# Performance work log

Measured on AMD Instinct MI355X. Metric: run time of the kernel, lower is better.

Reference implementation:

```python
import jax, jax.numpy as jnp
import numpy as np

# dims: B=32 batch, F=40 max_frames, NB=36 num_boxes, R=512 region size, H=512 hidden
# feat_size D = R + 2H = 1536 ; relation attn input = 2D = 3072

def _soft_attention(feats, hidden, Wf, bf, Wh, bh, wa):
    # feats: (N, L, Din), hidden: (N, H) -> att feat (N, Din), alpha (N, L)
    e = jnp.tanh(feats @ Wf.T + bf + (hidden @ Wh.T + bh)[:, None, :]) @ wa  # (N, L)
    alpha = jax.nn.softmax(e, axis=1)
    att = jnp.einsum('nl,nld->nd', alpha, feats)
    return att, alpha


def setup_inputs() -> dict:
    key = jax.random.key(0)
    ks = jax.random.split(key, 16)
    B, F, NB, R, H = 32, 40, 36, 512, 512
    D = R + 2 * H  # 1536
    s = 0.02
    inp = {
        'i3d_feats': jax.random.normal(ks[0], (B, F, 2 * H), jnp.float32),
        'object_feats': jax.random.normal(ks[1], (B, F, NB, R), jnp.float32),
        'hidden_state': jax.random.normal(ks[2], (B, H), jnp.float32),
        # spatial SoftAttention(R, H, H)
        'Ws_f': jax.random.normal(ks[3], (H, R), jnp.float32) * s,
        'bs_f': jnp.zeros((H,), jnp.float32),
        'Ws_h': jax.random.normal(ks[4], (H, H), jnp.float32) * s,
        'bs_h': jnp.zeros((H,), jnp.float32),
        'was': jax.random.normal(ks[5], (H,), jnp.float32) * s,
        # relation SoftAttention(2D, H, H)
        'Wr_f': jax.random.normal(ks[6], (H, 2 * D), jnp.float32) * s,
        'br_f': jnp.zeros((H,), jnp.float32),
        'Wr_h': jax.random.normal(ks[7], (H, H), jnp.float32) * s,
        'br_h': jnp.zeros((H,), jnp.float32),
        'war': jax.random.normal(ks[8], (H,), jnp.float32) * s,
    }
    return inp


def reference(i3d_feats, object_feats, hidden_state,
              Ws_f, bs_f, Ws_h, bs_h, was,
              Wr_f, br_f, Wr_h, br_h, war):
    B, F, NB, R = object_feats.shape
    # ---- spatial attention over boxes (per frame) ----
    feats = object_feats.reshape(B * F, NB, R)
    hidden_rep = jnp.repeat(hidden_state, F, axis=0)  # == hidden.repeat(1,F).reshape(B*F,-1)
    obj_att, _ = _soft_attention(feats, hidden_rep, Ws_f, bs_f, Ws_h, bs_h, was)
    obj_att = obj_att.reshape(B, F, R)
    feat = jnp.concatenate([obj_att, i3d_feats], axis=-1)  # (B, F, D)
    D = feat.shape[-1]
    # ---- relation attention over all F*F frame pairs ----
    # pairwise[b, i*F + j] = concat(feat[b, j], feat[b, i])  (feat1 varies fast, feat2 slow)
    # Decompose Wr_f @ concat(fj, fi) = Wr1 @ fj + Wr2 @ fi to avoid O(F^2 * 2D) tensor.
    Wr1, Wr2 = Wr_f[:, :D], Wr_f[:, D:]
    p1 = feat @ Wr1.T  # (B, F, H), applied to fast index j
    p2 = feat @ Wr2.T  # (B, F, H), applied to slow index i
    hproj = hidden_state @ Wr_h.T + br_h  # (B, H)
    e = jnp.tanh(p2[:, :, None, :] + p1[:, None, :, :] + (hproj + br_f)[:, None, None, :]) @ war  # (B,F,F) [i,j]
    alpha = jax.nn.softmax(e.reshape(B, F * F), axis=1).reshape(B, F, F)
    # weighted sum of concat(feat[j], feat[i]) splits into two marginal sums
    rel1 = jnp.einsum('bij,bjd->bd', alpha, feat)
    rel2 = jnp.einsum('bij,bid->bd', alpha, feat)
    return jnp.concatenate([rel1, rel2], axis=-1)  # (B, 2D)
```

## Files before the change

kernel.cpp:

```cpp
#include <hip/hip_runtime.h>
#include <stdint.h>

#define B_SZ 32
#define F_SZ 40
#define NB_SZ 36
#define R_SZ 512
#define H_SZ 512
#define D_SZ 1536
#define M1 (B_SZ * F_SZ * NB_SZ)
#define NROW (B_SZ * F_SZ)
#define FNB (F_SZ * NB_SZ)

typedef __attribute__((ext_vector_type(8))) short short8;
typedef __attribute__((ext_vector_type(4))) float f32x4;

__device__ __forceinline__ unsigned short f2bf(float f) {
    unsigned int x = __float_as_uint(f);
    return (unsigned short)((x + 0x7fffu + ((x >> 16) & 1u)) >> 16);
}
__device__ __forceinline__ float bf2f(unsigned short u) {
    union { unsigned int i; float f; } v; v.i = ((unsigned int)u) << 16; return v.f;
}
__device__ __forceinline__ unsigned int cvtpk(float lo, float hi) {
    unsigned int r;
    asm("v_cvt_pk_bf16_f32 %0, %1, %2" : "=v"(r) : "v"(lo), "v"(hi));
    return r;
}
__device__ __forceinline__ float fast_rcp(float x) {
    float r; asm("v_rcp_f32 %0, %1" : "=v"(r) : "v"(x)); return r;
}
__device__ __forceinline__ float fast_tanh(float x) {
    float t = __builtin_amdgcn_exp2f(2.8853900817779268f * x);
    return 1.0f - 2.0f * fast_rcp(t + 1.0f);
}

__device__ __forceinline__ void gload_lds16(const void* gsrc, void* ldst) {
    __builtin_amdgcn_global_load_lds(
        (const __attribute__((address_space(1))) unsigned int*)gsrc,
        (__attribute__((address_space(3))) unsigned int*)ldst, 16, 0, 0);
}

__global__ __launch_bounds__(256) void k_pre(
    const float* __restrict__ hidden,
    const float* __restrict__ Wsh, const float* __restrict__ bsh,
    const float* __restrict__ bsf,
    const float* __restrict__ Wrh, const float* __restrict__ brh,
    const float* __restrict__ brf,
    float* __restrict__ hs, float* __restrict__ hr,
    const float* __restrict__ Wsf, unsigned short* __restrict__ Wsb)
{
    const int t = threadIdx.x;
    if (blockIdx.x >= 256) {
        int i = ((blockIdx.x - 256) * 256 + t) * 8;
        float4 f0 = *(const float4*)(Wsf + i);
        float4 f1 = *(const float4*)(Wsf + i + 4);
        uint4 pk = {cvtpk(f0.x, f0.y), cvtpk(f0.z, f0.w),
                    cvtpk(f1.x, f1.y), cvtpk(f1.z, f1.w)};
        *(uint4*)(Wsb + i) = pk;
        return;
    }
    __shared__ float hid[H_SZ];
    const int b = blockIdx.x >> 3, hc = blockIdx.x & 7;
    for (int i = t; i < H_SZ; i += 256) hid[i] = hidden[b * H_SZ + i];
    __syncthreads();
    const int h = hc * 64 + (t >> 2), kq = t & 3;
    const float* r1 = Wsh + (size_t)h * H_SZ + kq * 128;
    const float* r2 = Wrh + (size_t)h * H_SZ + kq * 128;
    const float* hh = hid + kq * 128;
    float a1 = 0.f, a2 = 0.f;
    for (int k = 0; k < 128; k += 4) {
        float4 v1 = *(const float4*)(r1 + k);
        float4 v2 = *(const float4*)(r2 + k);
        a1 += hh[k] * v1.x + hh[k+1] * v1.y + hh[k+2] * v1.z + hh[k+3] * v1.w;
        a2 += hh[k] * v2.x + hh[k+1] * v2.y + hh[k+2] * v2.z + hh[k+3] * v2.w;
    }
    a1 += __shfl_xor(a1, 1); a1 += __shfl_xor(a1, 2);
    a2 += __shfl_xor(a2, 1); a2 += __shfl_xor(a2, 2);
    if (kq == 0) {
        hs[b * H_SZ + h] = a1 + bsh[h] + bsf[h];
        hr[b * H_SZ + h] = a2 + brh[h] + brf[h];
    }
}

__global__ __launch_bounds__(256, 3) void k_e1_mfma(
    const float* __restrict__ feats,
    const unsigned short* __restrict__ Wsb,
    const float* __restrict__ was,
    const float* __restrict__ hs,
    float* __restrict__ e1p)
{
    __shared__ __align__(16) unsigned char As[2][64 * 128];
    __shared__ __align__(16) unsigned char Bs[2][128 * 128];
    __shared__ float hsl[2][256];
    __shared__ float wasl[256];
    __shared__ float eps[2][64];

    const int bx = blockIdx.x;
    const int wid = (bx & 7) * 180 + (bx >> 3);
    const int mb = wid >> 1, by = wid & 1;
    const int m0 = mb * 64, hb = by * 256;
    const int t = threadIdx.x;
    const int b0 = m0 / FNB, b1 = (m0 + 63) / FNB;
    const int thr = (b0 + 1) * FNB - m0;

    if (t < 256) {
        hsl[0][t] = hs[b0 * H_SZ + hb + t];
        hsl[1][t] = hs[b1 * H_SZ + hb + t];
        wasl[t]   = was[hb + t];
    }

    const int lane = t & 63, w = t >> 6;
    const int wr = w >> 1, wc = w & 1;
    const int l15 = lane & 15, lk = lane >> 4;

    int ar[2], brw[4];
#pragma unroll
    for (int i = 0; i < 2; i++) ar[i] = wr * 32 + i * 16 + l15;
#pragma unroll
    for (int j = 0; j < 4; j++) brw[j] = wc * 64 + j * 16 + l15;

    const int srow = t >> 3;
    const int scol = t & 7;
    const int wub  = (t & 192) * 16;

    float4 alo[2], ahi[2];
    f32x4 acc[2][8] = {};
    float ep[2][4] = {{0.f}};

#define E1_LOAD_A(K0) do { \
    _Pragma("unroll") \
    for (int it = 0; it < 2; it++) { \
        int cid = it * 256 + t; \
        int r = cid >> 3, c = cid & 7; \
        const float* src = feats + (size_t)(m0 + r) * R_SZ + (K0) + c * 8; \
        alo[it] = *(const float4*)src; \
        ahi[it] = *(const float4*)(src + 4); \
    } } while (0)

#define E1_WRITE_A(AB) do { \
    _Pragma("unroll") \
    for (int it = 0; it < 2; it++) { \
        int cid = it * 256 + t; \
        int r = cid >> 3, c = cid & 7; \
        uint4 pk = {cvtpk(alo[it].x, alo[it].y), cvtpk(alo[it].z, alo[it].w), \
                    cvtpk(ahi[it].x, ahi[it].y), cvtpk(ahi[it].z, ahi[it].w)}; \
        *(uint4*)(&As[AB][r * 128 + ((c ^ (r & 7)) << 4)]) = pk; \
    } } while (0)

#define E1_STAGE_B(BUF, HP, K0) do { \
    _Pragma("unroll") \
    for (int it = 0; it < 4; it++) { \
        int r = it * 32 + srow; \
        int gc = scol ^ (r & 7); \
        gload_lds16(Wsb + (size_t)(hb + (HP) * 128 + r) * R_SZ + (K0) + gc * 8, \
                    &Bs[BUF][it * 4096 + wub]); \
    } } while (0)

#define E1_COMPUTE(HP, BB, AB) do { \
    _Pragma("unroll") \
    for (int ks = 0; ks < 2; ks++) { \
        short8 a[2], bv[4]; \
        int c = ks * 4 + lk; \
        _Pragma("unroll") \
        for (int i = 0; i < 2; i++) \
            a[i] = *(const short8*)(&As[AB][ar[i] * 128 + ((c ^ (ar[i] & 7)) << 4)]); \
        _Pragma("unroll") \
        for (int j = 0; j < 4; j++) \
            bv[j] = *(const short8*)(&Bs[BB][brw[j] * 128 + ((c ^ (brw[j] & 7)) << 4)]); \
        _Pragma("unroll") \
        for (int i = 0; i < 2; i++) \
        _Pragma("unroll") \
        for (int j = 0; j < 4; j++) \
            acc[i][(HP) * 4 + j] = __builtin_amdgcn_mfma_f32_16x16x32_bf16( \
                a[i], bv[j], acc[i][(HP) * 4 + j], 0, 0, 0); \
    } } while (0)

    E1_LOAD_A(0);
    E1_STAGE_B(0, 0, 0);
    E1_WRITE_A(0);
    __syncthreads();

    for (int ki = 0; ki < 8; ki++) {
        const int ab = ki & 1;
        E1_STAGE_B(1, 1, ki * 64);
        if (ki < 7) E1_LOAD_A((ki + 1) * 64);
        E1_COMPUTE(0, 0, ab);
        __syncthreads();
        if (ki < 7) E1_STAGE_B(0, 0, (ki + 1) * 64);
        E1_COMPUTE(1, 1, ab);
        if (ki < 7) E1_WRITE_A(ab ^ 1);
        __syncthreads();
    }

#pragma unroll
    for (int jj = 0; jj < 8; jj++) {
        int hl = (jj >> 2) * 128 + wc * 64 + (jj & 3) * 16 + l15;
        float wv = wasl[hl];
#pragma unroll
        for (int i = 0; i < 2; i++) {
#pragma unroll
            for (int q = 0; q < 4; q++) {
                int r = wr * 32 + i * 16 + lk * 4 + q;
                float hv = hsl[r >= thr ? 1 : 0][hl];
                ep[i][q] += fast_tanh(acc[i][jj][q] + hv) * wv;
            }
        }
    }
#pragma unroll
    for (int i = 0; i < 2; i++)
#pragma unroll
        for (int q = 0; q < 4; q++) {
            float v = ep[i][q];
            v += __shfl_xor(v, 1);
            v += __shfl_xor(v, 2);
            v += __shfl_xor(v, 4);
            v += __shfl_xor(v, 8);
            if (l15 == 0) eps[wc][wr * 32 + i * 16 + lk * 4 + q] = v;
        }
    __syncthreads();
    if (t < 64) e1p[(size_t)by * M1 + m0 + t] = eps[0][t] + eps[1][t];
#undef E1_LOAD_A
#undef E1_WRITE_A
#undef E1_STAGE_B
#undef E1_COMPUTE
}

__global__ __launch_bounds__(256) void k_softatt(
    const float* __restrict__ feats,
    const float* __restrict__ i3d,
    const float* __restrict__ e1p,
    unsigned short* __restrict__ feat)
{
    __shared__ float alpha[2][NB_SZ];
    const int n0 = blockIdx.x * 2;
    const int t = threadIdx.x;
    const int w = t >> 6;

    if (w < 2) {
        const int n = n0 + w, lane = t & 63;
        float v = -1e30f;
        if (lane < NB_SZ) {
            int idx = n * NB_SZ + lane;
            v = e1p[idx] + e1p[M1 + idx];
        }
        float m = v;
#pragma unroll
        for (int off = 32; off; off >>= 1) m = fmaxf(m, __shfl_xor(m, off));
        float ex = (lane < NB_SZ) ? __expf(v - m) : 0.f;
        float ssum = ex;
#pragma unroll
        for (int off = 32; off; off >>= 1) ssum += __shfl_xor(ssum, off);
        if (lane < NB_SZ) alpha[w][lane] = ex / ssum;
    }
    __syncthreads();

    const int g = t >> 7, lc = t & 127;
    const int n = n0 + g;
    float4 a4 = {0.f, 0.f, 0.f, 0.f};
    const float* base = feats + (size_t)n * NB_SZ * R_SZ + lc * 4;
    for (int ll = 0; ll < NB_SZ; ll++) {
        float al = alpha[g][ll];
        float4 pv = *(const float4*)(base + ll * R_SZ);
        a4.x += al * pv.x; a4.y += al * pv.y;
        a4.z += al * pv.z; a4.w += al * pv.w;
    }
    uint2 att = {cvtpk(a4.x, a4.y), cvtpk(a4.z, a4.w)};
    *(uint2*)(feat + (size_t)n * D_SZ + lc * 4) = att;

    const float* ib = i3d + (size_t)n * 1024 + lc * 8;
    float4 iv0 = *(const float4*)ib;
    float4 iv1 = *(const float4*)(ib + 4);
    uint4 pk = {cvtpk(iv0.x, iv0.y), cvtpk(iv0.z, iv0.w),
                cvtpk(iv1.x, iv1.y), cvtpk(iv1.z, iv1.w)};
    *(uint4*)(feat + (size_t)n * D_SZ + 512 + lc * 8) = pk;
}

__global__ __launch_bounds__(256) void k_pgemm_mfma(
    const unsigned short* __restrict__ feat,
    const float* __restrict__ Wrf,
    float* __restrict__ p)
{
    __shared__ __align__(16) unsigned char As[2][32 * 256];
    __shared__ __align__(16) unsigned char Bs[2][32 * 256];

    const int bx = blockIdx.x;
    const int wid = (bx & 7) * 160 + (bx >> 3);
    const int mb = wid % 40, nb = wid / 40;
    const int m0 = mb * 32, j0 = nb * 32;
    const int t = threadIdx.x;

    const int lane = t & 63, w = t >> 6;
    const int wrm = w >> 1, wcn = w & 1;
    const int l15 = lane & 15, lk = lane >> 4;

    const int arow = wrm * 16 + l15;
    const int brow = wcn * 16 + l15;

    const size_t brow_base = (j0 < 512) ? (size_t)j0 * 3072
                                        : ((size_t)(j0 - 512) * 3072 + 1536);

    float4 blo[2], bhi[2];
    f32x4 acc = {};

#define PG_STAGE_A(BUF, K0) do { \
    _Pragma("unroll") \
    for (int it = 0; it < 2; it++) { \
        int cid = it * 256 + t; \
        int r = cid >> 4, c = cid & 15; \
        int gc = c ^ (r & 7); \
        gload_lds16(feat + (size_t)(m0 + r) * D_SZ + (K0) + gc * 8, \
                    &As[BUF][it * 4096 + (t & 192) * 16]); \
    } } while (0)

#define PG_LOAD_B(K0) do { \
    _Pragma("unroll") \
    for (int it = 0; it < 2; it++) { \
        int cid = it * 256 + t; \
        int r = cid >> 4, c = cid & 15; \
        const float* src = Wrf + brow_base + (size_t)r * 3072 + (K0) + c * 8; \
        blo[it] = *(const float4*)src; \
        bhi[it] = *(const float4*)(src + 4); \
    } } while (0)

#define PG_WRITE_B(BUF) do { \
    _Pragma("unroll") \
    for (int it = 0; it < 2; it++) { \
        int cid = it * 256 + t; \
        int r = cid >> 4, c = cid & 15; \
        uint4 pk = {cvtpk(blo[it].x, blo[it].y), cvtpk(blo[it].z, blo[it].w), \
                    cvtpk(bhi[it].x, bhi[it].y), cvtpk(bhi[it].z, bhi[it].w)}; \
        *(uint4*)(&Bs[BUF][r * 256 + ((c ^ (r & 7)) << 4)]) = pk; \
    } } while (0)

#define PG_COMPUTE(BUF) do { \
    _Pragma("unroll") \
    for (int ks = 0; ks < 4; ks++) { \
        int c = ks * 4 + lk; \
        short8 av = *(const short8*)(&As[BUF][arow * 256 + ((c ^ (arow & 7)) << 4)]); \
        short8 bv = *(const short8*)(&Bs[BUF][brow * 256 + ((c ^ (brow & 7)) << 4)]); \
        acc = __builtin_amdgcn_mfma_f32_16x16x32_bf16(av, bv, acc, 0, 0, 0); \
    } } while (0)

    PG_LOAD_B(0);
    PG_STAGE_A(0, 0);
    PG_WRITE_B(0);
    __syncthreads();

#pragma unroll
    for (int ki = 0; ki < 12; ki++) {
        const int cur = ki & 1;
        if (ki < 11) {
            PG_LOAD_B((ki + 1) * 128);
            PG_STAGE_A(cur ^ 1, (ki + 1) * 128);
        }
        PG_COMPUTE(cur);
        if (ki < 11) PG_WRITE_B(cur ^ 1);
        __syncthreads();
    }

#pragma unroll
    for (int q = 0; q < 4; q++) {
        int row = m0 + wrm * 16 + lk * 4 + q;
        int col = j0 + wcn * 16 + l15;
        p[(size_t)row * 1024 + col] = acc[q];
    }
#undef PG_STAGE_A
#undef PG_LOAD_B
#undef PG_WRITE_B
#undef PG_COMPUTE
}

__global__ __launch_bounds__(256) void k_e2(
    const float* __restrict__ p,
    const float* __restrict__ hr,
    const float* __restrict__ war,
    float* __restrict__ e2)
{
    __shared__ float p1l[F_SZ][512];
    const int blk = blockIdx.x;
    const int b = blk / 10, io = blk % 10;
    const int t = threadIdx.x;
    const int w = t >> 6, l = t & 63;

#pragma unroll
    for (int u = 0; u < 10; u++) {
        int cid = u * 256 + t;
        int r = cid >> 6, c = cid & 63;
        const float* src = p + (size_t)(b * F_SZ + r) * 1024 + c * 8;
        *(float4*)&p1l[r][c * 8]     = *(const float4*)src;
        *(float4*)&p1l[r][c * 8 + 4] = *(const float4*)(src + 4);
    }

    const int i = io * 4 + w;
    const int ni = b * F_SZ + i;
    float base[8], warf[8];
    {
        float4 pa = *(const float4*)(p + (size_t)ni * 1024 + 512 + l * 8);
        float4 pb = *(const float4*)(p + (size_t)ni * 1024 + 512 + l * 8 + 4);
        float4 ha = *(const float4*)(hr + b * H_SZ + l * 8);
        float4 hb = *(const float4*)(hr + b * H_SZ + l * 8 + 4);
        base[0] = pa.x + ha.x; base[1] = pa.y + ha.y; base[2] = pa.z + ha.z; base[3] = pa.w + ha.w;
        base[4] = pb.x + hb.x; base[5] = pb.y + hb.y; base[6] = pb.z + hb.z; base[7] = pb.w + hb.w;
        float4 wa = *(const float4*)(war + l * 8);
        float4 wb = *(const float4*)(war + l * 8 + 4);
        warf[0] = wa.x; warf[1] = wa.y; warf[2] = wa.z; warf[3] = wa.w;
        warf[4] = wb.x; warf[5] = wb.y; warf[6] = wb.z; warf[7] = wb.w;
    }
    __syncthreads();

    for (int j = 0; j < F_SZ; j++) {
        const float* r = p1l[j];
        float4 va = *(const float4*)(r + l * 8);
        float4 vb = *(const float4*)(r + l * 8 + 4);
        float pv[8] = {va.x, va.y, va.z, va.w, vb.x, vb.y, vb.z, vb.w};
        float s = 0.f;
#pragma unroll
        for (int u = 0; u < 8; u++) s += fast_tanh(pv[u] + base[u]) * warf[u];
#pragma unroll
        for (int off = 32; off; off >>= 1) s += __shfl_xor(s, off);
        if (l == 0) e2[(size_t)b * 1600 + i * F_SZ + j] = s;
    }
}

__global__ __launch_bounds__(256) void k_out(
    const float* __restrict__ e2,
    const unsigned short* __restrict__ feat,
    float* __restrict__ out)
{
    __shared__ float alpha[1600];
    __shared__ float red[4];
    __shared__ float rs[F_SZ], cs[F_SZ];
    const int b = blockIdx.x >> 1, half = blockIdx.x & 1;
    const int t = threadIdx.x;
    const int w = t >> 6, l = t & 63;

    float lm = -1e30f;
    for (int idx = t; idx < 1600; idx += 256) {
        float v = e2[(size_t)b * 1600 + idx];
        alpha[idx] = v;
        lm = fmaxf(lm, v);
    }
#pragma unroll
    for (int off = 32; off; off >>= 1) lm = fmaxf(lm, __shfl_xor(lm, off));
    if (l == 0) red[w] = lm;
    __syncthreads();
    float M = fmaxf(fmaxf(red[0], red[1]), fmaxf(red[2], red[3]));
    __syncthreads();
    float ls = 0.f;
    for (int idx = t; idx < 1600; idx += 256) {
        float ex = __expf(alpha[idx] - M);
        alpha[idx] = ex;
        ls += ex;
    }
#pragma unroll
    for (int off = 32; off; off >>= 1) ls += __shfl_xor(ls, off);
    if (l == 0) red[w] = ls;
    __syncthreads();
    float inv = 1.f / (red[0] + red[1] + red[2] + red[3]);

    if (t < F_SZ) {
        float s = 0.f;
        for (int j = 0; j < F_SZ; j++) s += alpha[t * F_SZ + j];
        rs[t] = s * inv;
    } else if (t >= 128 && t < 128 + F_SZ) {
        int j = t - 128;
        float s = 0.f;
        for (int i2 = 0; i2 < F_SZ; i2++) s += alpha[i2 * F_SZ + j];
        cs[j] = s * inv;
    }
    __syncthreads();

    const int cb = half * 768;
    float a1[3] = {0.f, 0.f, 0.f};
    float a2[3] = {0.f, 0.f, 0.f};
    for (int r = 0; r < F_SZ; r++) {
        float w1 = cs[r], w2 = rs[r];
        const unsigned short* fr = feat + (size_t)(b * F_SZ + r) * D_SZ + cb;
#pragma unroll
        for (int u = 0; u < 3; u++) {
            float f = bf2f(fr[t + u * 256]);
            a1[u] += w1 * f;
            a2[u] += w2 * f;
        }
    }
#pragma unroll
    for (int u = 0; u < 3; u++) {
        out[(size_t)b * 3072 + cb + t + u * 256]        = a1[u];
        out[(size_t)b * 3072 + 1536 + cb + t + u * 256] = a2[u];
    }
}

extern "C" void kernel_launch(void* const* d_in, const int* in_sizes, int n_in,
                              void* d_out, int out_size, void* d_ws, size_t ws_size,
                              hipStream_t stream) {
    const float* i3d    = (const float*)d_in[0];
    const float* objf   = (const float*)d_in[1];
    const float* hidden = (const float*)d_in[2];
    const float* Wsf    = (const float*)d_in[3];
    const float* bsf    = (const float*)d_in[4];
    const float* Wsh    = (const float*)d_in[5];
    const float* bsh    = (const float*)d_in[6];
    const float* was    = (const float*)d_in[7];
    const float* Wrf    = (const float*)d_in[8];
    const float* brf    = (const float*)d_in[9];
    const float* Wrh    = (const float*)d_in[10];
    const float* brh    = (const float*)d_in[11];
    const float* war    = (const float*)d_in[12];
    float* out = (float*)d_out;

    char* ws = (char*)d_ws;
    float* hs  = (float*)(ws);
    float* hr  = (float*)(ws + 65536);
    float* p   = (float*)(ws + 131072);
    float* e1p = (float*)(ws + 131072);
    unsigned short* Wsb = (unsigned short*)(ws + 4849664);
    float* e2  = (float*)(ws + 5373952);
    unsigned short* feat = (unsigned short*)(ws + 5578752);

    k_pre<<<dim3(384), dim3(256), 0, stream>>>(hidden, Wsh, bsh, bsf, Wrh, brh, brf, hs, hr, Wsf, Wsb);
    k_e1_mfma<<<dim3(1440), dim3(256), 0, stream>>>(objf, Wsb, was, hs, e1p);
    k_softatt<<<dim3(640), dim3(256), 0, stream>>>(objf, i3d, e1p, feat);
    k_pgemm_mfma<<<dim3(1280), dim3(256), 0, stream>>>(feat, Wrf, p);
    k_e2<<<dim3(320), dim3(256), 0, stream>>>(p, hr, war, e2);
    k_out<<<dim3(64), dim3(256), 0, stream>>>(e2, feat, out);
}
```

Baseline: 273.5 us.

## Enlarge e1 and projection GEMM tiles to 512-thread blocks; split output in thirds

The spatial-attention score GEMM now runs 128-row tiles with 512 threads instead of 64-row tiles with 256, halving the grid. The relation projection GEMM moves from 32x32 to 64x64 tiles, with each warp computing two MFMA row fragments. Both changes aim to cut redundant weight and feature staging through shared memory and raise reuse per block. The cost is more LDS and registers per block, lower occupancy, and fewer blocks to spread across CUs. The final weighted-sum kernel splits each batch's columns into thirds instead of halves, giving it more blocks.

```diff
diff --git a/kernel.cpp b/kernel.cpp
--- a/kernel.cpp
+++ b/kernel.cpp
@@ -82,25 +82,25 @@
     }
 }
 
-__global__ __launch_bounds__(256, 3) void k_e1_mfma(
+__global__ __launch_bounds__(512, 2) void k_e1_mfma(
     const float* __restrict__ feats,
     const unsigned short* __restrict__ Wsb,
     const float* __restrict__ was,
     const float* __restrict__ hs,
     float* __restrict__ e1p)
 {
-    __shared__ __align__(16) unsigned char As[2][64 * 128];
+    __shared__ __align__(16) unsigned char As[2][128 * 128];
     __shared__ __align__(16) unsigned char Bs[2][128 * 128];
     __shared__ float hsl[2][256];
     __shared__ float wasl[256];
-    __shared__ float eps[2][64];
+    __shared__ float eps[2][128];
 
     const int bx = blockIdx.x;
-    const int wid = (bx & 7) * 180 + (bx >> 3);
+    const int wid = (bx & 7) * 90 + (bx >> 3);
     const int mb = wid >> 1, by = wid & 1;
-    const int m0 = mb * 64, hb = by * 256;
+    const int m0 = mb * 128, hb = by * 256;
     const int t = threadIdx.x;
-    const int b0 = m0 / FNB, b1 = (m0 + 63) / FNB;
+    const int b0 = m0 / FNB, b1 = (m0 + 127) / FNB;
     const int thr = (b0 + 1) * FNB - m0;
 
     if (t < 256) {
@@ -120,8 +120,7 @@
     for (int j = 0; j < 4; j++) brw[j] = wc * 64 + j * 16 + l15;
 
     const int srow = t >> 3;
-    const int scol = t & 7;
-    const int wub  = (t & 192) * 16;
+    const int wub  = (t & 448) * 16;
 
     float4 alo[2], ahi[2];
     f32x4 acc[2][8] = {};
@@ -130,7 +129,7 @@
 #define E1_LOAD_A(K0) do { \
     _Pragma("unroll") \
     for (int it = 0; it < 2; it++) { \
-        int cid = it * 256 + t; \
+        int cid = it * 512 + t; \
         int r = cid >> 3, c = cid & 7; \
         const float* src = feats + (size_t)(m0 + r) * R_SZ + (K0) + c * 8; \
         alo[it] = *(const float4*)src; \
@@ -140,7 +139,7 @@
 #define E1_WRITE_A(AB) do { \
     _Pragma("unroll") \
     for (int it = 0; it < 2; it++) { \
-        int cid = it * 256 + t; \
+        int cid = it * 512 + t; \
         int r = cid >> 3, c = cid & 7; \
         uint4 pk = {cvtpk(alo[it].x, alo[it].y), cvtpk(alo[it].z, alo[it].w), \
                     cvtpk(ahi[it].x, ahi[it].y), cvtpk(ahi[it].z, ahi[it].w)}; \
@@ -149,11 +148,11 @@
 
 #define E1_STAGE_B(BUF, HP, K0) do { \
     _Pragma("unroll") \
-    for (int it = 0; it < 4; it++) { \
-        int r = it * 32 + srow; \
-        int gc = scol ^ (r & 7); \
+    for (int it = 0; it < 2; it++) { \
+        int r = it * 64 + srow; \
+        int gc = (t & 7) ^ (r & 7); \
         gload_lds16(Wsb + (size_t)(hb + (HP) * 128 + r) * R_SZ + (K0) + gc * 8, \
-                    &Bs[BUF][it * 4096 + wub]); \
+                    &Bs[BUF][it * 8192 + wub]); \
     } } while (0)
 
 #define E1_COMPUTE(HP, BB, AB) do { \
@@ -218,7 +217,7 @@
             if (l15 == 0) eps[wc][wr * 32 + i * 16 + lk * 4 + q] = v;
         }
     __syncthreads();
-    if (t < 64) e1p[(size_t)by * M1 + m0 + t] = eps[0][t] + eps[1][t];
+    if (t < 128) e1p[(size_t)by * M1 + m0 + t] = eps[0][t] + eps[1][t];
 #undef E1_LOAD_A
 #undef E1_WRITE_A
 #undef E1_STAGE_B
@@ -275,47 +274,48 @@
     *(uint4*)(feat + (size_t)n * D_SZ + 512 + lc * 8) = pk;
 }
 
-__global__ __launch_bounds__(256) void k_pgemm_mfma(
+__global__ __launch_bounds__(512, 2) void k_pgemm_mfma(
     const unsigned short* __restrict__ feat,
     const float* __restrict__ Wrf,
     float* __restrict__ p)
 {
-    __shared__ __align__(16) unsigned char As[2][32 * 256];
-    __shared__ __align__(16) unsigned char Bs[2][32 * 256];
+    __shared__ __align__(16) unsigned char As[2][64 * 256];
+    __shared__ __align__(16) unsigned char Bs[2][64 * 256];
 
     const int bx = blockIdx.x;
-    const int wid = (bx & 7) * 160 + (bx >> 3);
-    const int mb = wid % 40, nb = wid / 40;
-    const int m0 = mb * 32, j0 = nb * 32;
+    const int wid = (bx & 7) * 40 + (bx >> 3);
+    const int mb = wid % 20, nb = wid / 20;
+    const int m0 = mb * 64, j0 = nb * 64;
     const int t = threadIdx.x;
 
     const int lane = t & 63, w = t >> 6;
-    const int wrm = w >> 1, wcn = w & 1;
+    const int wrm = w >> 2, wcn = w & 3;
     const int l15 = lane & 15, lk = lane >> 4;
 
-    const int arow = wrm * 16 + l15;
+    int arow[2];
+    arow[0] = wrm * 32 + l15; arow[1] = arow[0] + 16;
     const int brow = wcn * 16 + l15;
 
     const size_t brow_base = (j0 < 512) ? (size_t)j0 * 3072
                                         : ((size_t)(j0 - 512) * 3072 + 1536);
 
     float4 blo[2], bhi[2];
-    f32x4 acc = {};
+    f32x4 acc[2] = {};
 
 #define PG_STAGE_A(BUF, K0) do { \
     _Pragma("unroll") \
     for (int it = 0; it < 2; it++) { \
-        int cid = it * 256 + t; \
+        int cid = it * 512 + t; \
         int r = cid >> 4, c = cid & 15; \
         int gc = c ^ (r & 7); \
         gload_lds16(feat + (size_t)(m0 + r) * D_SZ + (K0) + gc * 8, \
-                    &As[BUF][it * 4096 + (t & 192) * 16]); \
+                    &As[BUF][it * 8192 + (t & 448) * 16]); \
     } } while (0)
 
 #define PG_LOAD_B(K0) do { \
     _Pragma("unroll") \
     for (int it = 0; it < 2; it++) { \
-        int cid = it * 256 + t; \
+        int cid = it * 512 + t; \
         int r = cid >> 4, c = cid & 15; \
         const float* src = Wrf + brow_base + (size_t)r * 3072 + (K0) + c * 8; \
         blo[it] = *(const float4*)src; \
@@ -325,7 +325,7 @@
 #define PG_WRITE_B(BUF) do { \
     _Pragma("unroll") \
     for (int it = 0; it < 2; it++) { \
-        int cid = it * 256 + t; \
+        int cid = it * 512 + t; \
         int r = cid >> 4, c = cid & 15; \
         uint4 pk = {cvtpk(blo[it].x, blo[it].y), cvtpk(blo[it].z, blo[it].w), \
                     cvtpk(bhi[it].x, bhi[it].y), cvtpk(bhi[it].z, bhi[it].w)}; \
@@ -336,9 +336,11 @@
     _Pragma("unroll") \
     for (int ks = 0; ks < 4; ks++) { \
         int c = ks * 4 + lk; \
-        short8 av = *(const short8*)(&As[BUF][arow * 256 + ((c ^ (arow & 7)) << 4)]); \
+        short8 a0 = *(const short8*)(&As[BUF][arow[0] * 256 + ((c ^ (arow[0] & 7)) << 4)]); \
+        short8 a1 = *(const short8*)(&As[BUF][arow[1] * 256 + ((c ^ (arow[1] & 7)) << 4)]); \
         short8 bv = *(const short8*)(&Bs[BUF][brow * 256 + ((c ^ (brow & 7)) << 4)]); \
-        acc = __builtin_amdgcn_mfma_f32_16x16x32_bf16(av, bv, acc, 0, 0, 0); \
+        acc[0] = __builtin_amdgcn_mfma_f32_16x16x32_bf16(a0, bv, acc[0], 0, 0, 0); \
+        acc[1] = __builtin_amdgcn_mfma_f32_16x16x32_bf16(a1, bv, acc[1], 0, 0, 0); \
     } } while (0)
 
     PG_LOAD_B(0);
@@ -359,11 +361,13 @@
     }
 
 #pragma unroll
-    for (int q = 0; q < 4; q++) {
-        int row = m0 + wrm * 16 + lk * 4 + q;
-        int col = j0 + wcn * 16 + l15;
-        p[(size_t)row * 1024 + col] = acc[q];
-    }
+    for (int i = 0; i < 2; i++)
+#pragma unroll
+        for (int q = 0; q < 4; q++) {
+            int row = m0 + wrm * 32 + i * 16 + lk * 4 + q;
+            int col = j0 + wcn * 16 + l15;
+            p[(size_t)row * 1024 + col] = acc[i][q];
+        }
 #undef PG_STAGE_A
 #undef PG_LOAD_B
 #undef PG_WRITE_B
@@ -430,7 +434,7 @@
     __shared__ float alpha[1600];
     __shared__ float red[4];
     __shared__ float rs[F_SZ], cs[F_SZ];
-    const int b = blockIdx.x >> 1, half = blockIdx.x & 1;
+    const int b = blockIdx.x / 3, third = blockIdx.x % 3;
     const int t = threadIdx.x;
     const int w = t >> 6, l = t & 63;
 
@@ -470,21 +474,21 @@
     }
     __syncthreads();
 
-    const int cb = half * 768;
-    float a1[3] = {0.f, 0.f, 0.f};
-    float a2[3] = {0.f, 0.f, 0.f};
+    const int cb = third * 512;
+    float a1[2] = {0.f, 0.f};
+    float a2[2] = {0.f, 0.f};
     for (int r = 0; r < F_SZ; r++) {
         float w1 = cs[r], w2 = rs[r];
         const unsigned short* fr = feat + (size_t)(b * F_SZ + r) * D_SZ + cb;
 #pragma unroll
-        for (int u = 0; u < 3; u++) {
+        for (int u = 0; u < 2; u++) {
             float f = bf2f(fr[t + u * 256]);
             a1[u] += w1 * f;
             a2[u] += w2 * f;
         }
     }
 #pragma unroll
-    for (int u = 0; u < 3; u++) {
+    for (int u = 0; u < 2; u++) {
         out[(size_t)b * 3072 + cb + t + u * 256]        = a1[u];
         out[(size_t)b * 3072 + 1536 + cb + t + u * 256] = a2[u];
     }
@@ -518,9 +522,9 @@
     unsigned short* feat = (unsigned short*)(ws + 5578752);
 
     k_pre<<<dim3(384), dim3(256), 0, stream>>>(hidden, Wsh, bsh, bsf, Wrh, brh, brf, hs, hr, Wsf, Wsb);
-    k_e1_mfma<<<dim3(1440), dim3(256), 0, stream>>>(objf, Wsb, was, hs, e1p);
+    k_e1_mfma<<<dim3(720), dim3(512), 0, stream>>>(objf, Wsb, was, hs, e1p);
     k_softatt<<<dim3(640), dim3(256), 0, stream>>>(objf, i3d, e1p, feat);
-    k_pgemm_mfma<<<dim3(1280), dim3(256), 0, stream>>>(feat, Wrf, p);
+    k_pgemm_mfma<<<dim3(320), dim3(512), 0, stream>>>(feat, Wrf, p);
     k_e2<<<dim3(320), dim3(256), 0, stream>>>(p, hr, war, e2);
-    k_out<<<dim3(64), dim3(256), 0, stream>>>(e2, feat, out);
-}
+    k_out<<<dim3(96), dim3(256), 0, stream>>>(e2, feat, out);
+}
```

Result: slower. 280.8 us (+2.7%).
